# Optimization experiments

Measured on AMD Instinct MI355X. Metric: run time of the kernel, lower is better.

## Reference

```python
import jax, jax.numpy as jnp
import numpy as np

B, SQ, SKV, D, H = 2, 2048, 2048, 1024, 16
DH = D // H


def setup_inputs() -> dict:
    key = jax.random.key(0)
    ks = jax.random.split(key, 4)
    s = 0.02
    return {
        "query_input": jax.random.normal(ks[0], (B, SQ, D), jnp.float32),
        "kv_input": jax.random.normal(ks[1], (B, SKV, D), jnp.float32),
        "Wq": jax.random.normal(ks[2], (D, D), jnp.float32) * s,
        "bq": jnp.zeros((D,), jnp.float32),
        "Wkv": jax.random.normal(ks[3], (D, 2 * D), jnp.float32) * s,
        "bkv": jnp.zeros((2 * D,), jnp.float32),
        "Wo": jax.random.normal(jax.random.fold_in(key, 7), (D, D), jnp.float32) * s,
        "bo": jnp.zeros((D,), jnp.float32),
    }


def reference(query_input, kv_input, Wq, bq, Wkv, bkv, Wo, bo):
    scale = 1.0 / jnp.sqrt(jnp.float32(DH))
    # Projections
    q = query_input @ Wq + bq                      # [B, SQ, D]
    kv = kv_input @ Wkv + bkv                      # [B, SKV, 2D]
    k, v = jnp.split(kv, 2, axis=-1)               # [B, SKV, D] each
    # Split heads: [B, H, S, DH]
    q = q.reshape(B, SQ, H, DH).transpose(0, 2, 1, 3)
    k = k.reshape(B, SKV, H, DH).transpose(0, 2, 1, 3)
    v = v.reshape(B, SKV, H, DH).transpose(0, 2, 1, 3)
    # Scores S = QK^T / sqrt(d_k)
    scores = jnp.einsum("bhqd,bhkd->bhqk", q, k) * scale
    attn = jax.nn.softmax(scores, axis=-1)
    out = jnp.einsum("bhqk,bhkd->bhqd", attn, v)   # [B, H, SQ, DH]
    out = out.transpose(0, 2, 1, 3).reshape(B, SQ, D)
    return out @ Wo + bo
```

## Files before the change

kernel.cpp:

```cpp
#include <hip/hip_runtime.h>

typedef unsigned short u16;
typedef unsigned int u32;
typedef __bf16 bf16x8 __attribute__((ext_vector_type(8)));
typedef __bf16 bf16x2 __attribute__((ext_vector_type(2)));
typedef float f32x4 __attribute__((ext_vector_type(4)));
typedef float f32x16 __attribute__((ext_vector_type(16)));

#define QSCALE 0.18033688011112f

__device__ __forceinline__ u16 f2bf(float f) {
  u32 u = __builtin_bit_cast(u32, f);
  u += 0x7fffu + ((u >> 16) & 1u);
  return (u16)(u >> 16);
}

__device__ __forceinline__ u32 pkbf(float a, float b) {
  bf16x2 t = {(__bf16)a, (__bf16)b};
  return __builtin_bit_cast(u32, t);
}

__device__ __forceinline__ bf16x8 as_bf16x8(uint4 v) {
  return __builtin_bit_cast(bf16x8, v);
}

__device__ __forceinline__ void async16(const void* g, void* l) {
  __builtin_amdgcn_global_load_lds(
      (__attribute__((address_space(1))) void*)(g),
      (__attribute__((address_space(3))) void*)(l), 16, 0, 0);
}

__global__ void prep_kernel(const float* __restrict__ xq, const float* __restrict__ xkv,
                            const float* __restrict__ Wq, const float* __restrict__ Wkv,
                            const float* __restrict__ Wo,
                            u16* __restrict__ Xq16, u16* __restrict__ Xkv16,
                            u16* __restrict__ WqT, u16* __restrict__ WkvT,
                            u16* __restrict__ WoT) {
  const int bid = blockIdx.x, tid = threadIdx.x;
  if (bid < 8192) {
    int i = bid * 256 + tid;
    const float* s; u16* d; int j;
    if (i < 1048576) { s = xq; d = Xq16; j = i; }
    else             { s = xkv; d = Xkv16; j = i - 1048576; }
    float4 v = ((const float4*)s)[j];
    ushort4 o;
    o.x = f2bf(v.x); o.y = f2bf(v.y); o.z = f2bf(v.z); o.w = f2bf(v.w);
    ((ushort4*)d)[j] = o;
    return;
  }
  const int b2 = bid - 8192;
  const int z = b2 >> 11, rem = b2 & 2047;
  const int by = rem >> 6, bx = rem & 63;
  const float* src; u16* dst; int Nd;
  if (z == 0)      { src = Wq;  dst = WqT;  Nd = 1024; }
  else if (z == 1) { src = Wkv; dst = WkvT; Nd = 2048; }
  else             { src = Wo;  dst = WoT;  Nd = 1024; }
  const int n0 = bx * 32, k0 = by * 32;
  if (n0 >= Nd) return;
  __shared__ float tile[32][33];
  const int tx = tid & 31, ty = tid >> 5;
#pragma unroll
  for (int j = 0; j < 4; ++j)
    tile[ty + 8 * j][tx] = src[(size_t)(k0 + ty + 8 * j) * Nd + n0 + tx];
  __syncthreads();
#pragma unroll
  for (int j = 0; j < 4; ++j)
    dst[(size_t)(n0 + ty + 8 * j) * 1024 + k0 + tx] = f2bf(tile[tx][ty + 8 * j]);
}

template <int MI>
static __device__ __forceinline__ void gemm_core(
    const u16* __restrict__ A, const u16* __restrict__ Bt, int m0,
    uint4* sA, uint4* sB, f32x4 (*acc)[4]) {
  const int tid = threadIdx.x;
  const int wv = tid >> 6, lane = tid & 63;
  const int quad = lane >> 4, l16 = lane & 15;
  const int wm = (wv >> 1) * (MI * 16), wn = (wv & 1) * 64;

  const int ib0 = wv * 128 + lane, ib1 = ib0 + 64;
  const int br0 = ib0 >> 2, bc0 = (ib0 & 3) ^ ((br0 >> 1) & 3);
  const int br1 = ib1 >> 2, bc1 = (ib1 & 3) ^ ((br1 >> 1) & 3);
  const u16* gB0 = Bt + (size_t)br0 * 1024 + bc0 * 8;
  const u16* gB1 = Bt + (size_t)br1 * 1024 + bc1 * 8;

  const int ia0 = wv * (MI * 32) + lane;
  const int ar0 = ia0 >> 2, ac0 = (ia0 & 3) ^ ((ar0 >> 1) & 3);
  const u16* gA0 = A + (size_t)(m0 + ar0) * 1024 + ac0 * 8;
  const int ia1 = ia0 + 64;
  const int ar1 = ia1 >> 2, ac1 = (ia1 & 3) ^ ((ar1 >> 1) & 3);
  const u16* gA1 = A + (size_t)(m0 + ar1) * 1024 + ac1 * 8;
  uint4* sAw = sA + wv * (MI * 32);
  uint4* sBw = sB + wv * 128;

  for (int k0 = 0; k0 < 1024; k0 += 32) {
    __syncthreads();
    async16(gA0 + k0, sAw);
    if (MI == 4) async16(gA1 + k0, sAw + 64);
    async16(gB0 + k0, sBw);
    async16(gB1 + k0, sBw + 64);
    __syncthreads();

    bf16x8 af[MI], bfr[4];
#pragma unroll
    for (int mi = 0; mi < MI; ++mi) {
      int r = wm + mi * 16 + l16;
      af[mi] = as_bf16x8(sA[r * 4 + (quad ^ ((r >> 1) & 3))]);
    }
#pragma unroll
    for (int ni = 0; ni < 4; ++ni) {
      int r = wn + ni * 16 + l16;
      bfr[ni] = as_bf16x8(sB[r * 4 + (quad ^ ((r >> 1) & 3))]);
    }
#pragma unroll
    for (int mi = 0; mi < MI; ++mi)
#pragma unroll
      for (int ni = 0; ni < 4; ++ni)
        acc[mi][ni] = __builtin_amdgcn_mfma_f32_16x16x32_bf16(
            af[mi], bfr[ni], acc[mi][ni], 0, 0, 0);
  }
}

__global__ __launch_bounds__(256, 3) void gemm_qkv(
    const u16* __restrict__ Xq, const u16* __restrict__ Xkv,
    const u16* __restrict__ WqT, const u16* __restrict__ WkvT,
    const float* __restrict__ bq, const float* __restrict__ bkv,
    u16* __restrict__ Qd, u16* __restrict__ Kd, u16* __restrict__ Vd) {
  __shared__ uint4 sA[512], sB[512];
  f32x4 acc[4][4] = {};
  const int n0 = blockIdx.x * 128, m0 = blockIdx.y * 128;
  const u16* A = (n0 < 1024) ? Xq : Xkv;
  const u16* Bt = (n0 < 1024) ? (WqT + (size_t)n0 * 1024)
                              : (WkvT + (size_t)(n0 - 1024) * 1024);
  const float* bias = (n0 < 1024) ? (bq + n0) : (bkv + (n0 - 1024));
  gemm_core<4>(A, Bt, m0, sA, sB, acc);

  const int tid = threadIdx.x, wv = tid >> 6, lane = tid & 63;
  const int quad = lane >> 4, l16 = lane & 15;
  const int wm = (wv >> 1) * 64, wn = (wv & 1) * 64;
  const int bb = m0 >> 11;
  const int gmb = m0 + wm + quad * 4;
  const int ssb = (m0 & 2047) + wm + quad * 4;
#pragma unroll
  for (int ni = 0; ni < 4; ++ni) {
    const int gn = n0 + wn + ni * 16 + l16;
    const float bvn = bias[wn + ni * 16 + l16];
    if (gn < 1024) {
      u16* base = Qd + gn;
#pragma unroll
      for (int mi = 0; mi < 4; ++mi)
#pragma unroll
        for (int r = 0; r < 4; ++r)
          base[(size_t)(gmb + mi * 16 + r) * 1024] = f2bf((acc[mi][ni][r] + bvn) * QSCALE);
    } else if (gn < 2048) {
      u16* base = Kd + (gn - 1024);
#pragma unroll
      for (int mi = 0; mi < 4; ++mi)
#pragma unroll
        for (int r = 0; r < 4; ++r)
          base[(size_t)(gmb + mi * 16 + r) * 1024] = f2bf(acc[mi][ni][r] + bvn);
    } else {
      const int col = gn - 2048, hh = col >> 6, dh = col & 63;
      u16* base = Vd + ((size_t)(bb * 16 + hh) * 64 + dh) * 2048 + ssb;
#pragma unroll
      for (int mi = 0; mi < 4; ++mi) {
        ushort4 o;
        o.x = f2bf(acc[mi][ni][0] + bvn);
        o.y = f2bf(acc[mi][ni][1] + bvn);
        o.z = f2bf(acc[mi][ni][2] + bvn);
        o.w = f2bf(acc[mi][ni][3] + bvn);
        *(ushort4*)(base + mi * 16) = o;
      }
    }
  }
}

__global__ __launch_bounds__(256, 1) void flash_attn(
    const u16* __restrict__ Q, const u16* __restrict__ K,
    const u16* __restrict__ V, u16* __restrict__ O) {
  __shared__ uint4 sK[2][512];
  __shared__ uint4 sV[2][512];
  __shared__ float sL[256];

  const int tid = threadIdx.x;
  const int wv = tid >> 6, lane = tid & 63;
  const int c = lane & 31, hh = lane >> 5;
  const int hb = blockIdx.x & 31;
  const int q0 = (blockIdx.x >> 5) * 256;
  const int h = hb & 15, bz = hb >> 4;

  const u16* Qb = Q + ((size_t)(bz * 2048 + q0 + wv * 64)) * 1024 + h * 64;
  const u16* Kb = K + ((size_t)(bz * 2048)) * 1024 + h * 64;
  const u16* Vb = V + ((size_t)(bz * 16 + h)) * 64 * 2048;

  const int i0 = wv * 128 + lane, i1 = i0 + 64;
  const int r0 = i0 >> 3, r1 = i1 >> 3;
  const int ck0 = (i0 & 7) ^ (r0 & 7), ck1 = (i1 & 7) ^ (r1 & 7);
  const u16* gK0 = Kb + (size_t)r0 * 1024 + ck0 * 8;
  const u16* gK1 = Kb + (size_t)r1 * 1024 + ck1 * 8;
  const u16* gV0 = Vb + (size_t)r0 * 2048 + ck0 * 8;
  const u16* gV1 = Vb + (size_t)r1 * 2048 + ck1 * 8;
  const int wo = wv * 128;

  bf16x8 qf[2][4];
#pragma unroll
  for (int g = 0; g < 2; ++g) {
    const u16* qr = Qb + (size_t)(32 * g + c) * 1024 + hh * 8;
#pragma unroll
    for (int s = 0; s < 4; ++s)
      qf[g][s] = as_bf16x8(*(const uint4*)(qr + 16 * s));
  }

  f32x16 oacc[2][2] = {};
  float lp[2] = {0.f, 0.f};

  async16(gK0, &sK[0][wo]);
  async16(gK1, &sK[0][wo + 64]);
  async16(gV0, &sV[0][wo]);
  async16(gV1, &sV[0][wo + 64]);

  for (int t = 0; t < 32; ++t) {
    const int cur = t & 1;
    __syncthreads();
    if (t < 31) {
      const size_t ko = (size_t)(t + 1) * 64 * 1024;
      const int vo = (t + 1) * 64;
      async16(gK0 + ko, &sK[cur ^ 1][wo]);
      async16(gK1 + ko, &sK[cur ^ 1][wo + 64]);
      async16(gV0 + vo, &sV[cur ^ 1][wo]);
      async16(gV1 + vo, &sV[cur ^ 1][wo + 64]);
    }
    const uint4* K_ = sK[cur];
    const uint4* V_ = sV[cur];

    bf16x8 kf[2][4], vf[2][4];
#pragma unroll
    for (int b = 0; b < 2; ++b) {
      const int row = 32 * b + c, sw = row & 7;
#pragma unroll
      for (int s = 0; s < 4; ++s) {
        kf[b][s] = as_bf16x8(K_[row * 8 + ((2 * s + hh) ^ sw)]);
        vf[b][s] = as_bf16x8(V_[row * 8 + ((2 * s + hh) ^ sw)]);
      }
    }

    bf16x8 pa[2][4];
#pragma unroll
    for (int b = 0; b < 2; ++b)
#pragma unroll
      for (int g = 0; g < 2; ++g) {
        f32x16 sAcc = {};
#pragma unroll
        for (int s = 0; s < 4; ++s)
          sAcc = __builtin_amdgcn_mfma_f32_32x32x16_bf16(kf[b][s], qf[g][s], sAcc, 0, 0, 0);
        float e[16];
#pragma unroll
        for (int r = 0; r < 16; ++r) e[r] = __builtin_amdgcn_exp2f(sAcc[r]);
        float t0 = (e[0] + e[1]) + (e[2] + e[3]);
        float t1 = (e[4] + e[5]) + (e[6] + e[7]);
        float t2 = (e[8] + e[9]) + (e[10] + e[11]);
        float t3 = (e[12] + e[13]) + (e[14] + e[15]);
        lp[g] += (t0 + t1) + (t2 + t3);
        u32 wA0 = pkbf(e[0], e[1]),   wA1 = pkbf(e[2], e[3]);
        u32 wB0 = pkbf(e[4], e[5]),   wB1 = pkbf(e[6], e[7]);
        u32 wC0 = pkbf(e[8], e[9]),   wC1 = pkbf(e[10], e[11]);
        u32 wD0 = pkbf(e[12], e[13]), wD1 = pkbf(e[14], e[15]);
        asm("v_permlane32_swap_b32 %0, %1" : "+v"(wA0), "+v"(wB0));
        asm("v_permlane32_swap_b32 %0, %1" : "+v"(wA1), "+v"(wB1));
        asm("v_permlane32_swap_b32 %0, %1" : "+v"(wC0), "+v"(wD0));
        asm("v_permlane32_swap_b32 %0, %1" : "+v"(wC1), "+v"(wD1));
        uint4 f0 = {wA0, wA1, wB0, wB1};
        uint4 f1 = {wC0, wC1, wD0, wD1};
        pa[g][2 * b]     = as_bf16x8(f0);
        pa[g][2 * b + 1] = as_bf16x8(f1);
      }

#pragma unroll
    for (int g = 0; g < 2; ++g)
#pragma unroll
      for (int nb = 0; nb < 2; ++nb)
#pragma unroll
        for (int ks = 0; ks < 4; ++ks)
          oacc[g][nb] = __builtin_amdgcn_mfma_f32_32x32x16_bf16(
              pa[g][ks], vf[nb][ks], oacc[g][nb], 0, 0, 0);
  }

#pragma unroll
  for (int g = 0; g < 2; ++g) {
    u32 a = __builtin_bit_cast(u32, lp[g]);
    u32 b = a;
    asm("v_permlane32_swap_b32 %0, %1" : "+v"(a), "+v"(b));
    float tot = __builtin_bit_cast(float, a) + __builtin_bit_cast(float, b);
    sL[wv * 64 + 32 * g + c] = 1.0f / tot;
  }

#pragma unroll
  for (int g = 0; g < 2; ++g) {
    u16* Ob = O + ((size_t)(bz * 2048 + q0 + wv * 64 + 32 * g)) * 1024 + h * 64;
#pragma unroll
    for (int nb = 0; nb < 2; ++nb)
#pragma unroll
      for (int r = 0; r < 16; ++r) {
        const int qr = (r & 3) + 8 * (r >> 2) + 4 * hh;
        float rl = sL[wv * 64 + 32 * g + qr];
        Ob[(size_t)qr * 1024 + nb * 32 + c] = f2bf(oacc[g][nb][r] * rl);
      }
  }
}

__global__ __launch_bounds__(256, 2) void gemm_out(
    const u16* __restrict__ A, const u16* __restrict__ Bt,
    const float* __restrict__ bias, float* __restrict__ C) {
  __shared__ uint4 sA[256], sB[512];
  f32x4 acc[2][4] = {};
  const int n0 = blockIdx.x * 128, m0 = blockIdx.y * 64;
  gemm_core<2>(A, Bt + (size_t)n0 * 1024, m0, sA, sB, acc);

  const int tid = threadIdx.x, wv = tid >> 6, lane = tid & 63;
  const int quad = lane >> 4, l16 = lane & 15;
  const int wm = (wv >> 1) * 32, wn = (wv & 1) * 64;
  float bv[4];
#pragma unroll
  for (int ni = 0; ni < 4; ++ni) bv[ni] = bias[n0 + wn + ni * 16 + l16];
#pragma unroll
  for (int mi = 0; mi < 2; ++mi)
#pragma unroll
    for (int ni = 0; ni < 4; ++ni)
#pragma unroll
      for (int r = 0; r < 4; ++r) {
        int gm = m0 + wm + mi * 16 + quad * 4 + r;
        int gn = n0 + wn + ni * 16 + l16;
        C[(size_t)gm * 1024 + gn] = acc[mi][ni][r] + bv[ni];
      }
}

extern "C" void kernel_launch(void* const* d_in, const int* in_sizes, int n_in,
                              void* d_out, int out_size, void* d_ws, size_t ws_size,
                              hipStream_t stream) {
  const float* xq  = (const float*)d_in[0];
  const float* xkv = (const float*)d_in[1];
  const float* Wq  = (const float*)d_in[2];
  const float* bq  = (const float*)d_in[3];
  const float* Wkv = (const float*)d_in[4];
  const float* bkv = (const float*)d_in[5];
  const float* Wo  = (const float*)d_in[6];
  const float* bo  = (const float*)d_in[7];
  float* out = (float*)d_out;

  char* p = (char*)d_ws;
  u16* Xq16  = (u16*)p; p += (size_t)8 << 20;
  u16* Xkv16 = (u16*)p; p += (size_t)8 << 20;
  u16* WqT   = (u16*)p; p += (size_t)2 << 20;
  u16* WkvT  = (u16*)p; p += (size_t)4 << 20;
  u16* WoT   = (u16*)p; p += (size_t)2 << 20;
  u16* Q16   = (u16*)p; p += (size_t)8 << 20;
  u16* K16   = (u16*)p; p += (size_t)8 << 20;
  u16* Vt16  = (u16*)p; p += (size_t)8 << 20;
  u16* O16   = (u16*)p; p += (size_t)8 << 20;

  prep_kernel<<<14336, 256, 0, stream>>>(xq, xkv, Wq, Wkv, Wo,
                                         Xq16, Xkv16, WqT, WkvT, WoT);
  gemm_qkv<<<dim3(24, 32), 256, 0, stream>>>(Xq16, Xkv16, WqT, WkvT, bq, bkv,
                                             Q16, K16, Vt16);
  flash_attn<<<256, 256, 0, stream>>>(Q16, K16, Vt16, O16);
  gemm_out<<<dim3(8, 64), 256, 0, stream>>>(O16, WoT, bo, out);
}
```

Baseline: 210.7 us.

## Split KV sequence across two wave groups per attention block with LDS reduction

```diff
diff --git a/kernel.cpp b/kernel.cpp
--- a/kernel.cpp
+++ b/kernel.cpp
@@ -174,32 +174,35 @@
   }
 }
 
-__global__ __launch_bounds__(256, 1) void flash_attn(
+__global__ __launch_bounds__(512, 2) void flash_attn(
     const u16* __restrict__ Q, const u16* __restrict__ K,
     const u16* __restrict__ V, u16* __restrict__ O) {
-  __shared__ uint4 sK[2][512];
-  __shared__ uint4 sV[2][512];
-  __shared__ float sL[256];
+  __shared__ uint4 sK[2][2][512];
+  __shared__ uint4 sV[2][2][512];
+  __shared__ float sO[16384];
+  __shared__ float sLB[256];
+  __shared__ float sLA[256];
 
   const int tid = threadIdx.x;
   const int wv = tid >> 6, lane = tid & 63;
+  const int grp = wv >> 2, wq = wv & 3;
   const int c = lane & 31, hh = lane >> 5;
   const int hb = blockIdx.x & 31;
   const int q0 = (blockIdx.x >> 5) * 256;
   const int h = hb & 15, bz = hb >> 4;
 
-  const u16* Qb = Q + ((size_t)(bz * 2048 + q0 + wv * 64)) * 1024 + h * 64;
-  const u16* Kb = K + ((size_t)(bz * 2048)) * 1024 + h * 64;
-  const u16* Vb = V + ((size_t)(bz * 16 + h)) * 64 * 2048;
-
-  const int i0 = wv * 128 + lane, i1 = i0 + 64;
+  const u16* Qb = Q + ((size_t)(bz * 2048 + q0 + wq * 64)) * 1024 + h * 64;
+  const u16* Kb = K + ((size_t)(bz * 2048 + grp * 64)) * 1024 + h * 64;
+  const u16* Vb = V + ((size_t)(bz * 16 + h)) * 64 * 2048 + grp * 64;
+
+  const int i0 = wq * 128 + lane, i1 = i0 + 64;
   const int r0 = i0 >> 3, r1 = i1 >> 3;
   const int ck0 = (i0 & 7) ^ (r0 & 7), ck1 = (i1 & 7) ^ (r1 & 7);
   const u16* gK0 = Kb + (size_t)r0 * 1024 + ck0 * 8;
   const u16* gK1 = Kb + (size_t)r1 * 1024 + ck1 * 8;
   const u16* gV0 = Vb + (size_t)r0 * 2048 + ck0 * 8;
   const u16* gV1 = Vb + (size_t)r1 * 2048 + ck1 * 8;
-  const int wo = wv * 128;
+  const int wo = wq * 128;
 
   bf16x8 qf[2][4];
 #pragma unroll
@@ -213,24 +216,24 @@
   f32x16 oacc[2][2] = {};
   float lp[2] = {0.f, 0.f};
 
-  async16(gK0, &sK[0][wo]);
-  async16(gK1, &sK[0][wo + 64]);
-  async16(gV0, &sV[0][wo]);
-  async16(gV1, &sV[0][wo + 64]);
-
-  for (int t = 0; t < 32; ++t) {
+  async16(gK0, &sK[grp][0][wo]);
+  async16(gK1, &sK[grp][0][wo + 64]);
+  async16(gV0, &sV[grp][0][wo]);
+  async16(gV1, &sV[grp][0][wo + 64]);
+
+  for (int t = 0; t < 16; ++t) {
     const int cur = t & 1;
     __syncthreads();
-    if (t < 31) {
-      const size_t ko = (size_t)(t + 1) * 64 * 1024;
-      const int vo = (t + 1) * 64;
-      async16(gK0 + ko, &sK[cur ^ 1][wo]);
-      async16(gK1 + ko, &sK[cur ^ 1][wo + 64]);
-      async16(gV0 + vo, &sV[cur ^ 1][wo]);
-      async16(gV1 + vo, &sV[cur ^ 1][wo + 64]);
-    }
-    const uint4* K_ = sK[cur];
-    const uint4* V_ = sV[cur];
+    if (t < 15) {
+      const size_t ko = (size_t)(t + 1) * 128 * 1024;
+      const int vo = (t + 1) * 128;
+      async16(gK0 + ko, &sK[grp][cur ^ 1][wo]);
+      async16(gK1 + ko, &sK[grp][cur ^ 1][wo + 64]);
+      async16(gV0 + vo, &sV[grp][cur ^ 1][wo]);
+      async16(gV1 + vo, &sV[grp][cur ^ 1][wo + 64]);
+    }
+    const uint4* K_ = sK[grp][cur];
+    const uint4* V_ = sV[grp][cur];
 
     bf16x8 kf[2][4], vf[2][4];
 #pragma unroll
@@ -284,26 +287,54 @@
               pa[g][ks], vf[nb][ks], oacc[g][nb], 0, 0, 0);
   }
 
+  float rtot[2];
 #pragma unroll
   for (int g = 0; g < 2; ++g) {
     u32 a = __builtin_bit_cast(u32, lp[g]);
     u32 b = a;
     asm("v_permlane32_swap_b32 %0, %1" : "+v"(a), "+v"(b));
-    float tot = __builtin_bit_cast(float, a) + __builtin_bit_cast(float, b);
-    sL[wv * 64 + 32 * g + c] = 1.0f / tot;
-  }
-
-#pragma unroll
-  for (int g = 0; g < 2; ++g) {
-    u16* Ob = O + ((size_t)(bz * 2048 + q0 + wv * 64 + 32 * g)) * 1024 + h * 64;
-#pragma unroll
-    for (int nb = 0; nb < 2; ++nb)
-#pragma unroll
-      for (int r = 0; r < 16; ++r) {
-        const int qr = (r & 3) + 8 * (r >> 2) + 4 * hh;
-        float rl = sL[wv * 64 + 32 * g + qr];
-        Ob[(size_t)qr * 1024 + nb * 32 + c] = f2bf(oacc[g][nb][r] * rl);
-      }
+    rtot[g] = __builtin_bit_cast(float, a) + __builtin_bit_cast(float, b);
+  }
+
+  if (grp) {
+#pragma unroll
+    for (int g = 0; g < 2; ++g) {
+      sLB[wq * 64 + 32 * g + c] = rtot[g];
+#pragma unroll
+      for (int nb = 0; nb < 2; ++nb) {
+        float* dst = sO + (wq * 4 + g * 2 + nb) * 1024;
+#pragma unroll
+        for (int r = 0; r < 16; ++r)
+          dst[r * 64 + lane] = oacc[g][nb][r];
+      }
+    }
+  }
+  __syncthreads();
+  if (!grp) {
+#pragma unroll
+    for (int g = 0; g < 2; ++g) {
+#pragma unroll
+      for (int nb = 0; nb < 2; ++nb) {
+        const float* srcp = sO + (wq * 4 + g * 2 + nb) * 1024;
+#pragma unroll
+        for (int r = 0; r < 16; ++r)
+          oacc[g][nb][r] += srcp[r * 64 + lane];
+      }
+      float tot = rtot[g] + sLB[wq * 64 + 32 * g + c];
+      sLA[wq * 64 + 32 * g + c] = 1.0f / tot;
+    }
+#pragma unroll
+    for (int g = 0; g < 2; ++g) {
+      u16* Ob = O + ((size_t)(bz * 2048 + q0 + wq * 64 + 32 * g)) * 1024 + h * 64;
+#pragma unroll
+      for (int nb = 0; nb < 2; ++nb)
+#pragma unroll
+        for (int r = 0; r < 16; ++r) {
+          const int qr = (r & 3) + 8 * (r >> 2) + 4 * hh;
+          float rl = sLA[wq * 64 + 32 * g + qr];
+          Ob[(size_t)qr * 1024 + nb * 32 + c] = f2bf(oacc[g][nb][r] * rl);
+        }
+    }
   }
 }
 
@@ -361,6 +392,6 @@
                                          Xq16, Xkv16, WqT, WkvT, WoT);
   gemm_qkv<<<dim3(24, 32), 256, 0, stream>>>(Xq16, Xkv16, WqT, WkvT, bq, bkv,
                                              Q16, K16, Vt16);
-  flash_attn<<<256, 256, 0, stream>>>(Q16, K16, Vt16, O16);
+  flash_attn<<<256, 512, 0, stream>>>(Q16, K16, Vt16, O16);
   gemm_out<<<dim3(8, 64), 256, 0, stream>>>(O16, WoT, bo, out);
 }
```

Result: faster. 195.4 us (-7.3%).
